# Kernel optimization log

Hardware: AMD Instinct MI355X
Metric: run time of the kernel (lower is better)

## Reference

```python
import jax, jax.numpy as jnp
import numpy as np

D, H, F, N, V, B, S, T = 512, 8, 2048, 2, 32000, 2, 1024, 1024


def _pe(seq_len, d):
    pos = np.arange(seq_len)[:, None].astype(np.float32)
    div = np.exp(np.arange(0, d, 2).astype(np.float32) * (-np.log(10000.0) / d))
    pe = np.zeros((seq_len, d), np.float32)
    pe[:, 0::2] = np.sin(pos * div)
    pe[:, 1::2] = np.cos(pos * div)
    return jnp.asarray(pe)


def _ln(x, g, b, eps=1e-6):
    # torch .var() default is unbiased (ddof=1)
    m = x.mean(-1, keepdims=True)
    v = jnp.sum((x - m) ** 2, -1, keepdims=True) / (x.shape[-1] - 1)
    return g * (x - m) / jnp.sqrt(v + eps) + b


def _mha(q, k, v, mask, w, b):
    # w: [4, D, D] (q,k,v,o); b: [4, D]
    Bq, Sq, Dm = q.shape
    Sk = k.shape[1]
    dk = Dm // H
    Q = (q @ w[0] + b[0]).reshape(Bq, Sq, H, dk).transpose(0, 2, 1, 3)
    K = (k @ w[1] + b[1]).reshape(Bq, Sk, H, dk).transpose(0, 2, 1, 3)
    Vv = (v @ w[2] + b[2]).reshape(Bq, Sk, H, dk).transpose(0, 2, 1, 3)
    s = jnp.einsum('bhqd,bhkd->bhqk', Q, K) / jnp.sqrt(jnp.float32(dk))
    s = jnp.where(mask == 0, jnp.float32(-1e9), s)
    a = jax.nn.softmax(s, axis=-1)
    o = jnp.einsum('bhqk,bhkd->bhqd', a, Vv).transpose(0, 2, 1, 3).reshape(Bq, Sq, Dm)
    return o @ w[3] + b[3]


def _ffn(x, w1, b1, w2, b2):
    return jax.nn.relu(x @ w1 + b1) @ w2 + b2


def _forward(src, tgt, src_mask, tgt_mask, p):
    (src_emb, tgt_emb, ea_w, ea_b, ef_w1, ef_b1, ef_w2, ef_b2, eln_g, eln_b, en_g, en_b,
     ds_w, ds_b, dc_w, dc_b, df_w1, df_b1, df_w2, df_b2, dln_g, dln_b, dn_g, dn_b, pw, pb) = p
    scale = jnp.sqrt(jnp.float32(D))
    # encoder
    x = src_emb[src] * scale + _pe(src.shape[1], D)
    for i in range(N):
        h = _ln(x, eln_g[i, 0], eln_b[i, 0])
        x = x + _mha(h, h, h, src_mask, ea_w[i], ea_b[i])
        h = _ln(x, eln_g[i, 1], eln_b[i, 1])
        x = x + _ffn(h, ef_w1[i], ef_b1[i], ef_w2[i], ef_b2[i])
    enc = _ln(x, en_g, en_b)
    # decoder
    y = tgt_emb[tgt] * scale + _pe(tgt.shape[1], D)
    for i in range(N):
        h = _ln(y, dln_g[i, 0], dln_b[i, 0])
        y = y + _mha(h, h, h, tgt_mask, ds_w[i], ds_b[i])
        h = _ln(y, dln_g[i, 1], dln_b[i, 1])
        y = y + _mha(h, enc, enc, src_mask, dc_w[i], dc_b[i])
        h = _ln(y, dln_g[i, 2], dln_b[i, 2])
        y = y + _ffn(h, df_w1[i], df_b1[i], df_w2[i], df_b2[i])
    y = _ln(y, dn_g, dn_b)
    return jax.nn.log_softmax(y @ pw + pb, axis=-1)


def setup_inputs() -> dict:
    key = jax.random.key(0)
    c = [0]
    def nk():
        c[0] += 1
        return jax.random.fold_in(key, c[0])
    def w(*s):
        return jax.random.normal(nk(), s, jnp.float32) * 0.02
    inp = {
        'src': jax.random.randint(nk(), (B, S), 0, V, jnp.int32),
        'tgt': jax.random.randint(nk(), (B, T), 0, V, jnp.int32),
        'src_mask': jnp.ones((B, 1, 1, S), jnp.int32),
        'tgt_mask': jnp.tril(jnp.ones((T, T), jnp.int32))[None, None],
        'src_emb': w(V, D), 'tgt_emb': w(V, D),
        'enc_attn_w': w(N, 4, D, D), 'enc_attn_b': jnp.zeros((N, 4, D), jnp.float32),
        'enc_ffn_w1': w(N, D, F), 'enc_ffn_b1': jnp.zeros((N, F), jnp.float32),
        'enc_ffn_w2': w(N, F, D), 'enc_ffn_b2': jnp.zeros((N, D), jnp.float32),
        'enc_ln_g': jnp.ones((N, 2, D), jnp.float32), 'enc_ln_b': jnp.zeros((N, 2, D), jnp.float32),
        'enc_norm_g': jnp.ones((D,), jnp.float32), 'enc_norm_b': jnp.zeros((D,), jnp.float32),
        'dec_self_w': w(N, 4, D, D), 'dec_self_b': jnp.zeros((N, 4, D), jnp.float32),
        'dec_cross_w': w(N, 4, D, D), 'dec_cross_b': jnp.zeros((N, 4, D), jnp.float32),
        'dec_ffn_w1': w(N, D, F), 'dec_ffn_b1': jnp.zeros((N, F), jnp.float32),
        'dec_ffn_w2': w(N, F, D), 'dec_ffn_b2': jnp.zeros((N, D), jnp.float32),
        'dec_ln_g': jnp.ones((N, 3, D), jnp.float32), 'dec_ln_b': jnp.zeros((N, 3, D), jnp.float32),
        'dec_norm_g': jnp.ones((D,), jnp.float32), 'dec_norm_b': jnp.zeros((D,), jnp.float32),
        'proj_w': w(D, V), 'proj_b': jnp.zeros((V,), jnp.float32),
    }
    return inp


def reference(src, tgt, src_mask, tgt_mask, src_emb, tgt_emb, enc_attn_w, enc_attn_b,
              enc_ffn_w1, enc_ffn_b1, enc_ffn_w2, enc_ffn_b2, enc_ln_g, enc_ln_b,
              enc_norm_g, enc_norm_b, dec_self_w, dec_self_b, dec_cross_w, dec_cross_b,
              dec_ffn_w1, dec_ffn_b1, dec_ffn_w2, dec_ffn_b2, dec_ln_g, dec_ln_b,
              dec_norm_g, dec_norm_b, proj_w, proj_b):
    p = (src_emb, tgt_emb, enc_attn_w, enc_attn_b, enc_ffn_w1, enc_ffn_b1, enc_ffn_w2,
         enc_ffn_b2, enc_ln_g, enc_ln_b, enc_norm_g, enc_norm_b, dec_self_w, dec_self_b,
         dec_cross_w, dec_cross_b, dec_ffn_w1, dec_ffn_b1, dec_ffn_w2, dec_ffn_b2,
         dec_ln_g, dec_ln_b, dec_norm_g, dec_norm_b, proj_w, proj_b)
    return _forward(src, tgt, src_mask, tgt_mask, p)
```

## Files before the change

kernel.cpp:

```cpp
#include <hip/hip_runtime.h>
#include <hip/hip_bf16.h>
#include <math.h>

using bf16 = __hip_bfloat16;
typedef float f32x4 __attribute__((ext_vector_type(4)));
typedef short short8 __attribute__((ext_vector_type(8)));

constexpr int kD = 512, kH = 8, kDk = 64, kF = 2048, kV = 32000;
constexpr int kB = 2, kS = 1024, kM = 2048, kBH = 16;

enum { ST_F32 = 0, ST_BF16, ST_QKV };

__device__ __forceinline__ void gload_lds16(const void* g, void* l) {
  __builtin_amdgcn_global_load_lds(
      (const __attribute__((address_space(1))) void*)g,
      (__attribute__((address_space(3))) void*)l, 16, 0, 0);
}

__device__ __forceinline__ float bfu2f(short u) {
  union { unsigned int i; float f; } c;
  c.i = ((unsigned int)(unsigned short)u) << 16;
  return c.f;
}

template <int BM, int BN, int STM, bool BIAS, bool RELU, bool RES, int NBUF, bool XSWZ, bool ASEL>
__launch_bounds__(256)
__global__ void k_gemm(const bf16* __restrict__ A, int lda, long long Az,
                       const bf16* __restrict__ Bt, int ldb, long long Bz,
                       void* __restrict__ Cv, int ldc, long long Cz,
                       int K, float alpha,
                       const float* __restrict__ bias,
                       const float* __restrict__ res,
                       const bf16* __restrict__ A2) {
  static_assert(NBUF == 1 || (BM == 64 && BN == 64), "pipeline path sized for 64x64");
  constexpr int FM = BM / 32, FN = BN / 32;
  __shared__ __attribute__((aligned(16))) bf16 As[NBUF][BM * 64];
  __shared__ __attribute__((aligned(16))) bf16 Bs[NBUF][BN * 64];
  const int tid = threadIdx.x;
  const int w = tid >> 6, lane = tid & 63;
  int bx = blockIdx.x, by = blockIdx.y;
  if constexpr (XSWZ) {
    const int nx = gridDim.x, ny = gridDim.y;
    const int lin = by * nx + bx;
    const int cpx = (nx * ny) >> 3;
    const int s = (lin & 7) * cpx + (lin >> 3);
    bx = s / ny;
    by = s - bx * ny;
  }
  const int bm = by * BM, bn = bx * BN;
  const int z = blockIdx.z;
  if constexpr (ASEL) { if (bn >= 512) A = A2; }
  A += (long long)z * Az;
  Bt += (long long)z * Bz;
  const int l15 = lane & 15, lhi = lane >> 4;
  const int wr = (w >> 1) * (BM / 2), wc = (w & 1) * (BN / 2);
  f32x4 acc[FM][FN] = {};
  const int nkt = K >> 6;

  auto stage = [&](int kt, int nb) {
#pragma unroll
    for (int it = 0; it < BM / 32; ++it) {
      int chunk = (it * 4 + w) * 64 + lane;
      int row = chunk >> 3, c = chunk & 7;
      int col = (c ^ (row & 7)) << 3;
      gload_lds16(A + (size_t)(bm + row) * lda + kt * 64 + col, As[nb] + (it * 4 + w) * 512);
    }
#pragma unroll
    for (int it = 0; it < BN / 32; ++it) {
      int chunk = (it * 4 + w) * 64 + lane;
      int row = chunk >> 3, c = chunk & 7;
      int col = (c ^ (row & 7)) << 3;
      gload_lds16(Bt + (size_t)(bn + row) * ldb + kt * 64 + col, Bs[nb] + (it * 4 + w) * 512);
    }
  };
  auto compute = [&](int cb) {
#pragma unroll
    for (int kk = 0; kk < 2; ++kk) {
      short8 af[FM], bf[FN];
#pragma unroll
      for (int i = 0; i < FM; ++i) {
        int row = wr + i * 16 + l15;
        af[i] = *(const short8*)(As[cb] + row * 64 + (((kk * 4 + lhi) ^ (row & 7)) * 8));
      }
#pragma unroll
      for (int j = 0; j < FN; ++j) {
        int row = wc + j * 16 + l15;
        bf[j] = *(const short8*)(Bs[cb] + row * 64 + (((kk * 4 + lhi) ^ (row & 7)) * 8));
      }
#pragma unroll
      for (int i = 0; i < FM; ++i)
#pragma unroll
        for (int j = 0; j < FN; ++j)
          acc[i][j] = __builtin_amdgcn_mfma_f32_16x16x32_bf16(af[i], bf[j], acc[i][j], 0, 0, 0);
    }
  };

  if constexpr (NBUF == 3) {
    stage(0, 0);
    stage(1, 1);
    stage(2, 2);
    asm volatile("s_waitcnt vmcnt(8)" ::: "memory");
    __builtin_amdgcn_s_barrier();
    __builtin_amdgcn_sched_barrier(0);
    int cur = 0;
    for (int kt = 0; kt < nkt; ++kt) {
      compute(cur);
      asm volatile("s_waitcnt lgkmcnt(0)" ::: "memory");
      __builtin_amdgcn_sched_barrier(0);
      if (kt + 1 < nkt) {
        __builtin_amdgcn_s_barrier();
        if (kt + 3 < nkt) {
          stage(kt + 3, cur);
          asm volatile("s_waitcnt vmcnt(8)" ::: "memory");
        } else {
          asm volatile("s_waitcnt vmcnt(0)" ::: "memory");
        }
        __builtin_amdgcn_s_barrier();
        __builtin_amdgcn_sched_barrier(0);
      }
      cur = (cur == 2) ? 0 : cur + 1;
    }
  } else {
    for (int kt = 0; kt < nkt; ++kt) {
      stage(kt, 0);
      __syncthreads();
      compute(0);
      __syncthreads();
    }
  }

#pragma unroll
  for (int i = 0; i < FM; ++i) {
#pragma unroll
    for (int j = 0; j < FN; ++j) {
#pragma unroll
      for (int r = 0; r < 4; ++r) {
        int m = bm + wr + i * 16 + lhi * 4 + r;
        int n = bn + wc + j * 16 + l15;
        float val = acc[i][j][r] * alpha;
        if constexpr (BIAS) val += bias[n];
        if constexpr (RELU) val = fmaxf(val, 0.f);
        if constexpr (RES) val += res[(size_t)m * ldc + n];
        if constexpr (STM == ST_F32) {
          ((float*)Cv)[(size_t)z * Cz + (size_t)m * ldc + n] = val;
        } else if constexpr (STM == ST_BF16) {
          ((bf16*)Cv)[(size_t)z * Cz + (size_t)m * ldc + n] = __float2bfloat16(val);
        } else if constexpr (STM == ST_QKV) {
          int seg = n >> 9, nn = n & 511;
          int b_ = m >> 10, s_ = m & 1023, h_ = nn >> 6, d_ = nn & 63;
          size_t idx = (seg < 2)
              ? (((size_t)(b_ * kH + h_) << 10) + s_) * kDk + d_
              : ((size_t)(b_ * kH + h_) * kDk + d_) * kS + s_;
          ((bf16*)Cv)[(size_t)seg * 1048576 + idx] = __float2bfloat16(val);
        }
      }
    }
  }
}

template <bool CAUSAL>
__launch_bounds__(256)
__global__ void k_fattn(const bf16* __restrict__ Q, const bf16* __restrict__ K,
                        const bf16* __restrict__ Vt, bf16* __restrict__ O) {
  __shared__ __attribute__((aligned(16))) bf16 Ks[3][4096];
  __shared__ __attribute__((aligned(16))) bf16 Vs[3][4096];
  __shared__ __attribute__((aligned(16))) bf16 Ps[4][1024];
  const int tid = threadIdx.x, w = tid >> 6, lane = tid & 63;
  const int l15 = lane & 15, lhi = lane >> 4;
  const int q0 = blockIdx.x * 64, bh = blockIdx.y;
  const int qw = q0 + w * 16;
  const bf16* Qp = Q + (((size_t)(bh << 10)) + qw + l15) * kDk;
  short8 aq[2];
  aq[0] = *(const short8*)(Qp + lhi * 8);
  aq[1] = *(const short8*)(Qp + 32 + lhi * 8);
  const int srow = w * 8 + (lane >> 3);
  const int sc = (lane & 7) ^ (srow & 7);
  const bf16* Ksrc = K + (((size_t)(bh << 10)) + srow) * kDk + sc * 8;
  const bf16* Vsrc = Vt + ((size_t)bh * kDk + srow) * kS + sc * 8;
  const int nt = CAUSAL ? (q0 >> 6) + 1 : (kS >> 6);

  auto stage = [&](int t, int nb) {
    int kv0 = t << 6;
    gload_lds16(Ksrc + (size_t)kv0 * kDk, Ks[nb] + w * 512);
    gload_lds16(Ksrc + (size_t)(kv0 + 32) * kDk, Ks[nb] + 2048 + w * 512);
    gload_lds16(Vsrc + kv0, Vs[nb] + w * 512);
    gload_lds16(Vsrc + kv0 + 32 * kS, Vs[nb] + 2048 + w * 512);
  };

  float m_[4], l_[4];
#pragma unroll
  for (int r = 0; r < 4; ++r) { m_[r] = -1e30f; l_[r] = 0.f; }
  f32x4 ao[4] = {};

  stage(0, 0);
  if (nt > 2) {
    stage(1, 1);
    stage(2, 2);
    asm volatile("s_waitcnt vmcnt(8)" ::: "memory");
  } else if (nt > 1) {
    stage(1, 1);
    asm volatile("s_waitcnt vmcnt(4)" ::: "memory");
  } else {
    asm volatile("s_waitcnt vmcnt(0)" ::: "memory");
  }
  __builtin_amdgcn_s_barrier();
  __builtin_amdgcn_sched_barrier(0);

  int cur = 0;
  for (int t = 0; t < nt; ++t) {
    f32x4 as[4] = {};
#pragma unroll
    for (int kk = 0; kk < 2; ++kk) {
      short8 bk[4];
#pragma unroll
      for (int nf = 0; nf < 4; ++nf) {
        int row = nf * 16 + l15;
        int c = (4 * kk + lhi) ^ (row & 7);
        bk[nf] = *(const short8*)(Ks[cur] + row * 64 + c * 8);
      }
#pragma unroll
      for (int nf = 0; nf < 4; ++nf)
        as[nf] = __builtin_amdgcn_mfma_f32_16x16x32_bf16(aq[kk], bk[nf], as[nf], 0, 0, 0);
    }
    float s[4][4];
#pragma unroll
    for (int nf = 0; nf < 4; ++nf)
#pragma unroll
      for (int r = 0; r < 4; ++r) {
        float v = as[nf][r] * 0.125f;
        if (CAUSAL && t == nt - 1) {
          int col = (t << 6) + nf * 16 + l15;
          int row = qw + lhi * 4 + r;
          if (col > row) v = -1e30f;
        }
        s[nf][r] = v;
      }
    float mn[4], scl[4], rsum[4];
#pragma unroll
    for (int r = 0; r < 4; ++r) {
      float mx = fmaxf(fmaxf(s[0][r], s[1][r]), fmaxf(s[2][r], s[3][r]));
      mx = fmaxf(mx, __shfl_xor(mx, 1));
      mx = fmaxf(mx, __shfl_xor(mx, 2));
      mx = fmaxf(mx, __shfl_xor(mx, 4));
      mx = fmaxf(mx, __shfl_xor(mx, 8));
      mn[r] = fmaxf(m_[r], mx);
      scl[r] = __expf(m_[r] - mn[r]);
      rsum[r] = 0.f;
    }
#pragma unroll
    for (int nf = 0; nf < 4; ++nf)
#pragma unroll
      for (int r = 0; r < 4; ++r) {
        float p = __expf(s[nf][r] - mn[r]);
        rsum[r] += p;
        int pr = lhi * 4 + r;
        int c = (2 * nf + (l15 >> 3)) ^ (pr & 7);
        Ps[w][pr * 64 + c * 8 + (l15 & 7)] = __float2bfloat16(p);
      }
#pragma unroll
    for (int r = 0; r < 4; ++r) {
      float su = rsum[r];
      su += __shfl_xor(su, 1);
      su += __shfl_xor(su, 2);
      su += __shfl_xor(su, 4);
      su += __shfl_xor(su, 8);
      l_[r] = l_[r] * scl[r] + su;
      m_[r] = mn[r];
    }
#pragma unroll
    for (int nf = 0; nf < 4; ++nf)
#pragma unroll
      for (int r = 0; r < 4; ++r) ao[nf][r] *= scl[r];
    asm volatile("s_waitcnt lgkmcnt(0)" ::: "memory");
    __builtin_amdgcn_sched_barrier(0);
#pragma unroll
    for (int kk = 0; kk < 2; ++kk) {
      short8 pa = *(const short8*)(Ps[w] + l15 * 64 + (((4 * kk + lhi) ^ (l15 & 7)) * 8));
      short8 bv[4];
#pragma unroll
      for (int nf = 0; nf < 4; ++nf) {
        int row = nf * 16 + l15;
        int c = (4 * kk + lhi) ^ (row & 7);
        bv[nf] = *(const short8*)(Vs[cur] + row * 64 + c * 8);
      }
#pragma unroll
      for (int nf = 0; nf < 4; ++nf)
        ao[nf] = __builtin_amdgcn_mfma_f32_16x16x32_bf16(pa, bv[nf], ao[nf], 0, 0, 0);
    }
    asm volatile("s_waitcnt lgkmcnt(0)" ::: "memory");
    __builtin_amdgcn_sched_barrier(0);
    if (t + 1 < nt) {
      __builtin_amdgcn_s_barrier();
      if (t + 3 < nt) {
        stage(t + 3, cur);
        asm volatile("s_waitcnt vmcnt(8)" ::: "memory");
      } else {
        asm volatile("s_waitcnt vmcnt(0)" ::: "memory");
      }
      __builtin_amdgcn_s_barrier();
      __builtin_amdgcn_sched_barrier(0);
    }
    cur = (cur == 2) ? 0 : cur + 1;
  }
  const int b_ = bh >> 3, h_ = bh & 7;
  float inv[4];
#pragma unroll
  for (int r = 0; r < 4; ++r) inv[r] = 1.f / l_[r];
#pragma unroll
  for (int nf = 0; nf < 4; ++nf)
#pragma unroll
    for (int r = 0; r < 4; ++r) {
      int q = qw + lhi * 4 + r;
      O[((size_t)(b_ * kS + q)) * kD + h_ * kDk + nf * 16 + l15] =
          __float2bfloat16(ao[nf][r] * inv[r]);
    }
}

struct TJobs {
  const float* src[8];
  bf16* dst[8];
  int K[8], N[8];
  int ofs[9];
};

__global__ void k_transpose_all(TJobs J) {
  __shared__ float t[32][33];
  const int tb = blockIdx.x;
  int j = 0;
#pragma unroll
  for (int i = 1; i < 8; ++i) j += (tb >= J.ofs[i]) ? 1 : 0;
  const int K = J.K[j], N = J.N[j];
  const int tn = N >> 5, tk = K >> 5;
  int r = tb - J.ofs[j];
  const int z = r / (tn * tk);
  r -= z * tn * tk;
  const int k0 = (r / tn) << 5, n0 = (r % tn) << 5;
  const float* Wp = J.src[j] + (size_t)z * K * N;
  bf16* WTp = J.dst[j] + (size_t)z * K * N;
  const int tx = threadIdx.x, ty = threadIdx.y;
#pragma unroll
  for (int rr = 0; rr < 32; rr += 8) t[ty + rr][tx] = Wp[(size_t)(k0 + ty + rr) * N + n0 + tx];
  __syncthreads();
#pragma unroll
  for (int rr = 0; rr < 32; rr += 8)
    WTp[(size_t)(n0 + ty + rr) * K + k0 + tx] = __float2bfloat16(t[tx][ty + rr]);
}

__global__ void k_embed2(const int* __restrict__ src, const int* __restrict__ tgt,
                         const float* __restrict__ se, const float* __restrict__ te,
                         float* __restrict__ xe, float* __restrict__ xd) {
  const int m = blockIdx.x, which = blockIdx.y;
  const int* tok = which ? tgt : src;
  const float* emb = which ? te : se;
  float* x = which ? xd : xe;
  int s = m & (kS - 1);
  const float* e = emb + (size_t)tok[m] * kD;
  float* xp = x + (size_t)m * kD;
  for (int d = threadIdx.x; d < kD; d += 256) {
    int i = d >> 1;
    float freq = __expf(-(float)(2 * i) * (9.210340371976184f / 512.0f));
    float ang = (float)s * freq;
    float pe = (d & 1) ? cosf(ang) : sinf(ang);
    xp[d] = e[d] * 22.62741699796952f + pe;
  }
}

__global__ void k_ln(const float* __restrict__ x, const float* __restrict__ g,
                     const float* __restrict__ b, bf16* __restrict__ out) {
  int w = threadIdx.x >> 6, lane = threadIdx.x & 63;
  int row = blockIdx.x * 4 + w;
  const float* xp = x + (size_t)row * kD;
  float v[8];
  float sum = 0.f;
#pragma unroll
  for (int i = 0; i < 8; ++i) { v[i] = xp[lane + i * 64]; sum += v[i]; }
#pragma unroll
  for (int o = 32; o; o >>= 1) sum += __shfl_xor(sum, o);
  float mean = sum * (1.f / 512.f);
  float sq = 0.f;
#pragma unroll
  for (int i = 0; i < 8; ++i) { float d = v[i] - mean; sq += d * d; }
#pragma unroll
  for (int o = 32; o; o >>= 1) sq += __shfl_xor(sq, o);
  float inv = rsqrtf(sq * (1.f / 511.f) + 1e-6f);
  bf16* op = out + (size_t)row * kD;
#pragma unroll
  for (int i = 0; i < 8; ++i) {
    int d = lane + i * 64;
    op[d] = __float2bfloat16(g[d] * (v[i] - mean) * inv + b[d]);
  }
}

__global__ __launch_bounds__(512, 1) void k_proj256(const bf16* __restrict__ A,
                                                    const bf16* __restrict__ Bt,
                                                    bf16* __restrict__ C,
                                                    const float* __restrict__ bias) {
  __shared__ __attribute__((aligned(16))) bf16 As[4][256 * 32];
  __shared__ __attribute__((aligned(16))) bf16 Bs[4][256 * 32];
  const int tid = threadIdx.x, w = tid >> 6, lane = tid & 63;
  const int l15 = lane & 15, lhi = lane >> 4;
  const int lin = blockIdx.y * 125 + blockIdx.x;
  const int s = (lin & 7) * 125 + (lin >> 3);
  const int bx = s >> 3, by = s & 7;
  const int bm = by * 256, bn = bx * 256;
  const int wr = (w >> 2) * 128, wc = (w & 3) * 64;
  const int rowq = tid >> 2, chk = tid & 3;
  const int swz = (chk ^ ((rowq >> 1) & 3)) << 3;
  const bf16* Asrc0 = A + (size_t)(bm + rowq) * kD + swz;
  const bf16* Asrc1 = A + (size_t)(bm + 128 + rowq) * kD + swz;
  const bf16* Bsrc0 = Bt + (size_t)(bn + rowq) * kD + swz;
  const bf16* Bsrc1 = Bt + (size_t)(bn + 128 + rowq) * kD + swz;
  const int ldsoff = w * 1024;

  auto stage = [&](int kt) {
    const int b = kt & 3;
    const int ko = kt * 32;
    gload_lds16(Asrc0 + ko, (char*)As[b] + ldsoff);
    gload_lds16(Asrc1 + ko, (char*)As[b] + 8192 + ldsoff);
    gload_lds16(Bsrc0 + ko, (char*)Bs[b] + ldsoff);
    gload_lds16(Bsrc1 + ko, (char*)Bs[b] + 8192 + ldsoff);
  };

  const int ra = wr + l15, rb = wc + l15;
  const int abase = ra * 64 + ((lhi ^ ((ra >> 1) & 3)) << 4);
  const int bbase = rb * 64 + ((lhi ^ ((rb >> 1) & 3)) << 4);

  f32x4 acc[8][4] = {};
  stage(0); stage(1); stage(2);
  for (int kt = 0; kt < 16; ++kt) {
    if (kt + 2 < 16)      asm volatile("s_waitcnt vmcnt(8)" ::: "memory");
    else if (kt + 1 < 16) asm volatile("s_waitcnt vmcnt(4)" ::: "memory");
    else                  asm volatile("s_waitcnt vmcnt(0)" ::: "memory");
    __builtin_amdgcn_s_barrier();
    __builtin_amdgcn_sched_barrier(0);
    if (kt + 3 < 16) stage(kt + 3);
    const int b = kt & 3;
    short8 af[8], bf[4];
#pragma unroll
    for (int i = 0; i < 8; ++i)
      af[i] = *(const short8*)((const char*)As[b] + abase + i * 1024);
#pragma unroll
    for (int j = 0; j < 4; ++j)
      bf[j] = *(const short8*)((const char*)Bs[b] + bbase + j * 1024);
#pragma unroll
    for (int i = 0; i < 8; ++i)
#pragma unroll
      for (int j = 0; j < 4; ++j)
        acc[i][j] = __builtin_amdgcn_mfma_f32_16x16x32_bf16(af[i], bf[j], acc[i][j], 0, 0, 0);
    asm volatile("s_waitcnt lgkmcnt(0)" ::: "memory");
    __builtin_amdgcn_sched_barrier(0);
  }
#pragma unroll
  for (int i = 0; i < 8; ++i)
#pragma unroll
    for (int j = 0; j < 4; ++j)
#pragma unroll
      for (int r = 0; r < 4; ++r) {
        int m = bm + wr + i * 16 + lhi * 4 + r;
        int n = bn + wc + j * 16 + l15;
        C[(size_t)m * kV + n] = __float2bfloat16(acc[i][j][r] + bias[n]);
      }
}

__global__ __launch_bounds__(640, 2) void k_lsm_bf(const bf16* __restrict__ L,
                                                   float* __restrict__ y) {
  const bf16* row = L + (size_t)blockIdx.x * kV;
  float* orow = y + (size_t)blockIdx.x * kV;
  const int t = threadIdx.x;
  const bool extra = t < 160;
  float v[56];
  float sum = 0.f;
#pragma unroll
  for (int i = 0; i < 6; ++i) {
    short8 s = *(const short8*)(row + (t + i * 640) * 8);
#pragma unroll
    for (int e = 0; e < 8; ++e) {
      float f = bfu2f(s[e]);
      v[i * 8 + e] = f;
      sum += __expf(f);
    }
  }
  if (extra) {
    short8 s = *(const short8*)(row + (3840 + t) * 8);
#pragma unroll
    for (int e = 0; e < 8; ++e) {
      float f = bfu2f(s[e]);
      v[48 + e] = f;
      sum += __expf(f);
    }
  }
#pragma unroll
  for (int o = 32; o; o >>= 1) sum += __shfl_xor(sum, o);
  __shared__ float red2[10];
  const int w = t >> 6, lane = t & 63;
  if (lane == 0) red2[w] = sum;
  __syncthreads();
  sum = 0.f;
#pragma unroll
  for (int i = 0; i < 10; ++i) sum += red2[i];
  const float sh = logf(sum);
#pragma unroll
  for (int i = 0; i < 6; ++i)
#pragma unroll
    for (int e = 0; e < 8; ++e) orow[(t + i * 640) * 8 + e] = v[i * 8 + e] - sh;
  if (extra)
#pragma unroll
    for (int e = 0; e < 8; ++e) orow[(3840 + t) * 8 + e] = v[48 + e] - sh;
}

extern "C" void kernel_launch(void* const* d_in, const int* in_sizes, int n_in,
                              void* d_out, int out_size, void* d_ws, size_t ws_size,
                              hipStream_t stream) {
  (void)in_sizes; (void)n_in; (void)out_size;
  if (ws_size < (size_t)212 * 1024 * 1024) return;

  const int* src = (const int*)d_in[0];
  const int* tgt = (const int*)d_in[1];
  const float* src_emb   = (const float*)d_in[4];
  const float* tgt_emb   = (const float*)d_in[5];
  const float* enc_attn_w = (const float*)d_in[6];
  const float* enc_attn_b = (const float*)d_in[7];
  const float* enc_ffn_w1 = (const float*)d_in[8];
  const float* enc_ffn_b1 = (const float*)d_in[9];
  const float* enc_ffn_w2 = (const float*)d_in[10];
  const float* enc_ffn_b2 = (const float*)d_in[11];
  const float* enc_ln_g  = (const float*)d_in[12];
  const float* enc_ln_b  = (const float*)d_in[13];
  const float* enc_norm_g = (const float*)d_in[14];
  const float* enc_norm_b = (const float*)d_in[15];
  const float* dec_self_w = (const float*)d_in[16];
  const float* dec_self_b = (const float*)d_in[17];
  const float* dec_cross_w = (const float*)d_in[18];
  const float* dec_cross_b = (const float*)d_in[19];
  const float* dec_ffn_w1 = (const float*)d_in[20];
  const float* dec_ffn_b1 = (const float*)d_in[21];
  const float* dec_ffn_w2 = (const float*)d_in[22];
  const float* dec_ffn_b2 = (const float*)d_in[23];
  const float* dec_ln_g  = (const float*)d_in[24];
  const float* dec_ln_b  = (const float*)d_in[25];
  const float* dec_norm_g = (const float*)d_in[26];
  const float* dec_norm_b = (const float*)d_in[27];
  const float* proj_w    = (const float*)d_in[28];
  const float* proj_b    = (const float*)d_in[29];

  char* ws = (char*)d_ws;
  auto MB = [](size_t x) { return x << 20; };
  bf16* enc_attn_wt  = (bf16*)(ws + MB(0));
  bf16* dec_self_wt  = (bf16*)(ws + MB(4));
  bf16* dec_cross_wt = (bf16*)(ws + MB(8));
  bf16* enc_f1t = (bf16*)(ws + MB(12));
  bf16* enc_f2t = (bf16*)(ws + MB(16));
  bf16* dec_f1t = (bf16*)(ws + MB(20));
  bf16* dec_f2t = (bf16*)(ws + MB(24));
  bf16* proj_wt = (bf16*)(ws + MB(28));
  float* x_enc  = (float*)(ws + MB(60));
  float* x_dec  = (float*)(ws + MB(64));
  bf16* hbuf    = (bf16*)(ws + MB(68));
  bf16* enc_bf  = (bf16*)(ws + MB(70));
  bf16* Qb      = (bf16*)(ws + MB(72));
  bf16* attn_o  = (bf16*)(ws + MB(78));
  bf16* logits  = (bf16*)(ws + MB(80));
  bf16* ffn_mid = (bf16*)d_out;

  TJobs tj;
  int acc = 0;
  auto setj = [&](int j, const float* s, bf16* d, int K, int N, int z) {
    tj.src[j] = s; tj.dst[j] = d; tj.K[j] = K; tj.N[j] = N; tj.ofs[j] = acc;
    acc += (K >> 5) * (N >> 5) * z;
  };
  setj(0, enc_attn_w, enc_attn_wt, 512, 512, 8);
  setj(1, dec_self_w, dec_self_wt, 512, 512, 8);
  setj(2, dec_cross_w, dec_cross_wt, 512, 512, 8);
  setj(3, enc_ffn_w1, enc_f1t, 512, 2048, 2);
  setj(4, enc_ffn_w2, enc_f2t, 2048, 512, 2);
  setj(5, dec_ffn_w1, dec_f1t, 512, 2048, 2);
  setj(6, dec_ffn_w2, dec_f2t, 2048, 512, 2);
  setj(7, proj_w, proj_wt, 512, 32000, 1);
  tj.ofs[8] = acc;
  k_transpose_all<<<acc, dim3(32, 8), 0, stream>>>(tj);

  k_embed2<<<dim3(kM, 2), 256, 0, stream>>>(src, tgt, src_emb, tgt_emb, x_enc, x_dec);

  auto LN = [&](const float* x, const float* g, const float* b, bf16* out) {
    k_ln<<<kM / 4, 256, 0, stream>>>(x, g, b, out);
  };
  auto out_proj = [&](const bf16* wt, const float* bias, float* xio) {
    k_gemm<64, 64, ST_F32, true, false, true, 3, false, false><<<dim3(8, 32, 1), 256, 0, stream>>>(
        attn_o, 512, 0, wt + 3 * 262144, 512, 0, xio, 512, 0, 512, 1.f, bias + 3 * 512, xio, nullptr);
  };
  auto self_attn = [&](const bf16* wt, const float* bias, bool causal, float* xio) {
    k_gemm<64, 64, ST_QKV, true, false, false, 3, false, false><<<dim3(24, 32, 1), 256, 0, stream>>>(
        hbuf, 512, 0, wt, 512, 0, Qb, 0, 0, 512, 1.f, bias, nullptr, nullptr);
    if (causal) k_fattn<true><<<dim3(16, kBH), 256, 0, stream>>>(Qb, Qb + 1048576, Qb + 2097152, attn_o);
    else        k_fattn<false><<<dim3(16, kBH), 256, 0, stream>>>(Qb, Qb + 1048576, Qb + 2097152, attn_o);
    out_proj(wt, bias, xio);
  };
  auto cross_attn = [&](const bf16* wt, const float* bias, float* xio) {
    k_gemm<64, 64, ST_QKV, true, false, false, 3, false, true><<<dim3(24, 32, 1), 256, 0, stream>>>(
        hbuf, 512, 0, wt, 512, 0, Qb, 0, 0, 512, 1.f, bias, nullptr, enc_bf);
    k_fattn<false><<<dim3(16, kBH), 256, 0, stream>>>(Qb, Qb + 1048576, Qb + 2097152, attn_o);
    out_proj(wt, bias, xio);
  };
  auto ffn_block = [&](float* xio, const bf16* w1t, const float* b1, const bf16* w2t,
                       const float* b2, const float* g, const float* bl) {
    LN(xio, g, bl, hbuf);
    k_gemm<64, 64, ST_BF16, true, true, false, 3, false, false><<<dim3(32, 32, 1), 256, 0, stream>>>(
        hbuf, 512, 0, w1t, 512, 0, ffn_mid, kF, 0, 512, 1.f, b1, nullptr, nullptr);
    k_gemm<64, 64, ST_F32, true, false, true, 3, false, false><<<dim3(8, 32, 1), 256, 0, stream>>>(
        ffn_mid, 2048, 0, w2t, 2048, 0, xio, 512, 0, 2048, 1.f, b2, xio, nullptr);
  };

  for (int i = 0; i < 2; ++i) {
    LN(x_enc, enc_ln_g + i * 1024, enc_ln_b + i * 1024, hbuf);
    self_attn(enc_attn_wt + (size_t)i * 1048576, enc_attn_b + i * 2048, false, x_enc);
    ffn_block(x_enc, enc_f1t + (size_t)i * 1048576, enc_ffn_b1 + i * 2048,
              enc_f2t + (size_t)i * 1048576, enc_ffn_b2 + i * 512,
              enc_ln_g + i * 1024 + 512, enc_ln_b + i * 1024 + 512);
  }
  LN(x_enc, enc_norm_g, enc_norm_b, enc_bf);

  for (int i = 0; i < 2; ++i) {
    LN(x_dec, dec_ln_g + i * 1536, dec_ln_b + i * 1536, hbuf);
    self_attn(dec_self_wt + (size_t)i * 1048576, dec_self_b + i * 2048, true, x_dec);
    LN(x_dec, dec_ln_g + i * 1536 + 512, dec_ln_b + i * 1536 + 512, hbuf);
    cross_attn(dec_cross_wt + (size_t)i * 1048576, dec_cross_b + i * 2048, x_dec);
    ffn_block(x_dec, dec_f1t + (size_t)i * 1048576, dec_ffn_b1 + i * 2048,
              dec_f2t + (size_t)i * 1048576, dec_ffn_b2 + i * 512,
              dec_ln_g + i * 1536 + 1024, dec_ln_b + i * 1536 + 1024);
  }
  LN(x_dec, dec_norm_g, dec_norm_b, hbuf);

  k_proj256<<<dim3(125, 8), 512, 0, stream>>>(hbuf, proj_wt, logits, proj_b);
  k_lsm_bf<<<kM, 640, 0, stream>>>(logits, (float*)d_out);
}
```

Measured before the change: 690.9 us.

## Fuse LayerNorm into residual GEMM epilogues and merge prep kernels

Each residual-output GEMM (attention out-projection and FFN down-projection) now counts finished column tiles per row block with an atomic counter. The last block to finish a row panel runs the following LayerNorm on those 64 rows, which removes the standalone LN launches. The weight transpose, embedding, and first encoder/decoder LayerNorms are merged into one prep kernel, with a second hbuf so the decoder's first LN can be done up front. The cost is a threadfence and atomic per block, a serialized LN tail on the last block of each row panel, and a memset for the counters.

```diff
diff --git a/kernel.cpp b/kernel.cpp
--- a/kernel.cpp
+++ b/kernel.cpp
@@ -23,7 +23,36 @@
   return c.f;
 }
 
-template <int BM, int BN, int STM, bool BIAS, bool RELU, bool RES, int NBUF, bool XSWZ, bool ASEL>
+__device__ __forceinline__ void ln4(int vb, const float* __restrict__ x,
+                                    const float* __restrict__ g,
+                                    const float* __restrict__ b,
+                                    bf16* __restrict__ out) {
+  int w = threadIdx.x >> 6, lane = threadIdx.x & 63;
+  int row = vb * 4 + w;
+  const float* xp = x + (size_t)row * kD;
+  float v[8];
+  float sum = 0.f;
+#pragma unroll
+  for (int i = 0; i < 8; ++i) { v[i] = xp[lane + i * 64]; sum += v[i]; }
+#pragma unroll
+  for (int o = 32; o; o >>= 1) sum += __shfl_xor(sum, o);
+  float mean = sum * (1.f / 512.f);
+  float sq = 0.f;
+#pragma unroll
+  for (int i = 0; i < 8; ++i) { float d = v[i] - mean; sq += d * d; }
+#pragma unroll
+  for (int o = 32; o; o >>= 1) sq += __shfl_xor(sq, o);
+  float inv = rsqrtf(sq * (1.f / 511.f) + 1e-6f);
+  bf16* op = out + (size_t)row * kD;
+#pragma unroll
+  for (int i = 0; i < 8; ++i) {
+    int d = lane + i * 64;
+    op[d] = __float2bfloat16(g[d] * (v[i] - mean) * inv + b[d]);
+  }
+}
+
+template <int BM, int BN, int STM, bool BIAS, bool RELU, bool RES, int NBUF, bool XSWZ,
+          bool ASEL, bool FUSELN>
 __launch_bounds__(256)
 __global__ void k_gemm(const bf16* __restrict__ A, int lda, long long Az,
                        const bf16* __restrict__ Bt, int ldb, long long Bz,
@@ -31,7 +60,11 @@
                        int K, float alpha,
                        const float* __restrict__ bias,
                        const float* __restrict__ res,
-                       const bf16* __restrict__ A2) {
+                       const bf16* __restrict__ A2,
+                       const float* __restrict__ lng,
+                       const float* __restrict__ lnb,
+                       bf16* __restrict__ lnout,
+                       unsigned* __restrict__ cnt) {
   static_assert(NBUF == 1 || (BM == 64 && BN == 64), "pipeline path sized for 64x64");
   constexpr int FM = BM / 32, FN = BN / 32;
   __shared__ __attribute__((aligned(16))) bf16 As[NBUF][BM * 64];
@@ -156,6 +189,23 @@
       }
     }
   }
+
+  if constexpr (FUSELN) {
+    __threadfence();
+    __syncthreads();
+    __shared__ int lastf;
+    if (tid == 0) {
+      unsigned v = __hip_atomic_fetch_add(&cnt[blockIdx.y], 1u,
+                                          __ATOMIC_ACQ_REL, __HIP_MEMORY_SCOPE_AGENT);
+      lastf = (v == gridDim.x - 1u) ? 1 : 0;
+    }
+    __syncthreads();
+    if (lastf) {
+      const float* xsrc = (const float*)Cv;
+#pragma unroll
+      for (int i = 0; i < BM / 4; ++i) ln4((bm >> 2) + i, xsrc, lng, lnb, lnout);
+    }
+  }
 }
 
 template <bool CAUSAL>
@@ -323,71 +373,83 @@
   int ofs[9];
 };
 
-__global__ void k_transpose_all(TJobs J) {
+struct PrepArgs {
+  TJobs tj; int ntile;
+  const int *src, *tgt;
+  const float *src_emb, *tgt_emb;
+  const float *eg, *eb, *dg, *db;
+  float *x_enc, *x_dec;
+  bf16 *hb_enc, *hb_dec;
+};
+
+__global__ void k_prep(PrepArgs P) {
   __shared__ float t[32][33];
-  const int tb = blockIdx.x;
-  int j = 0;
-#pragma unroll
-  for (int i = 1; i < 8; ++i) j += (tb >= J.ofs[i]) ? 1 : 0;
-  const int K = J.K[j], N = J.N[j];
-  const int tn = N >> 5, tk = K >> 5;
-  int r = tb - J.ofs[j];
-  const int z = r / (tn * tk);
-  r -= z * tn * tk;
-  const int k0 = (r / tn) << 5, n0 = (r % tn) << 5;
-  const float* Wp = J.src[j] + (size_t)z * K * N;
-  bf16* WTp = J.dst[j] + (size_t)z * K * N;
-  const int tx = threadIdx.x, ty = threadIdx.y;
-#pragma unroll
-  for (int rr = 0; rr < 32; rr += 8) t[ty + rr][tx] = Wp[(size_t)(k0 + ty + rr) * N + n0 + tx];
-  __syncthreads();
-#pragma unroll
-  for (int rr = 0; rr < 32; rr += 8)
-    WTp[(size_t)(n0 + ty + rr) * K + k0 + tx] = __float2bfloat16(t[tx][ty + rr]);
-}
-
-__global__ void k_embed2(const int* __restrict__ src, const int* __restrict__ tgt,
-                         const float* __restrict__ se, const float* __restrict__ te,
-                         float* __restrict__ xe, float* __restrict__ xd) {
-  const int m = blockIdx.x, which = blockIdx.y;
-  const int* tok = which ? tgt : src;
-  const float* emb = which ? te : se;
-  float* x = which ? xd : xe;
-  int s = m & (kS - 1);
+  __shared__ float red[4], red2[4];
+  const int tid = threadIdx.x;
+  if ((int)blockIdx.x < P.ntile) {
+    const int tb = blockIdx.x;
+    int j = 0;
+#pragma unroll
+    for (int i = 1; i < 8; ++i) j += (tb >= P.tj.ofs[i]) ? 1 : 0;
+    const int K = P.tj.K[j], N = P.tj.N[j];
+    const int tn = N >> 5, tk = K >> 5;
+    int r = tb - P.tj.ofs[j];
+    const int z = r / (tn * tk);
+    r -= z * tn * tk;
+    const int k0 = (r / tn) << 5, n0 = (r % tn) << 5;
+    const float* Wp = P.tj.src[j] + (size_t)z * K * N;
+    bf16* WTp = P.tj.dst[j] + (size_t)z * K * N;
+    const int tx = tid & 31, ty = tid >> 5;
+#pragma unroll
+    for (int rr = 0; rr < 32; rr += 8)
+      t[ty + rr][tx] = Wp[(size_t)(k0 + ty + rr) * N + n0 + tx];
+    __syncthreads();
+#pragma unroll
+    for (int rr = 0; rr < 32; rr += 8)
+      WTp[(size_t)(n0 + ty + rr) * K + k0 + tx] = __float2bfloat16(t[tx][ty + rr]);
+    return;
+  }
+  const int vb = blockIdx.x - P.ntile;
+  const int m = vb & (kM - 1), which = vb >> 11;
+  const int* tok = which ? P.tgt : P.src;
+  const float* emb = which ? P.tgt_emb : P.src_emb;
+  float* x = which ? P.x_dec : P.x_enc;
+  const int s = m & (kS - 1);
   const float* e = emb + (size_t)tok[m] * kD;
   float* xp = x + (size_t)m * kD;
-  for (int d = threadIdx.x; d < kD; d += 256) {
+  float v[2];
+#pragma unroll
+  for (int h = 0; h < 2; ++h) {
+    int d = tid + h * 256;
     int i = d >> 1;
     float freq = __expf(-(float)(2 * i) * (9.210340371976184f / 512.0f));
     float ang = (float)s * freq;
     float pe = (d & 1) ? cosf(ang) : sinf(ang);
-    xp[d] = e[d] * 22.62741699796952f + pe;
-  }
-}
-
-__global__ void k_ln(const float* __restrict__ x, const float* __restrict__ g,
-                     const float* __restrict__ b, bf16* __restrict__ out) {
-  int w = threadIdx.x >> 6, lane = threadIdx.x & 63;
-  int row = blockIdx.x * 4 + w;
-  const float* xp = x + (size_t)row * kD;
-  float v[8];
-  float sum = 0.f;
-#pragma unroll
-  for (int i = 0; i < 8; ++i) { v[i] = xp[lane + i * 64]; sum += v[i]; }
+    v[h] = e[d] * 22.62741699796952f + pe;
+    xp[d] = v[h];
+  }
+  const int w = tid >> 6, lane = tid & 63;
+  float sum = v[0] + v[1];
 #pragma unroll
   for (int o = 32; o; o >>= 1) sum += __shfl_xor(sum, o);
-  float mean = sum * (1.f / 512.f);
-  float sq = 0.f;
-#pragma unroll
-  for (int i = 0; i < 8; ++i) { float d = v[i] - mean; sq += d * d; }
+  if (lane == 0) red[w] = sum;
+  __syncthreads();
+  sum = red[0] + red[1] + red[2] + red[3];
+  const float mean = sum * (1.f / 512.f);
+  float sq = (v[0] - mean) * (v[0] - mean) + (v[1] - mean) * (v[1] - mean);
 #pragma unroll
   for (int o = 32; o; o >>= 1) sq += __shfl_xor(sq, o);
-  float inv = rsqrtf(sq * (1.f / 511.f) + 1e-6f);
-  bf16* op = out + (size_t)row * kD;
-#pragma unroll
-  for (int i = 0; i < 8; ++i) {
-    int d = lane + i * 64;
-    op[d] = __float2bfloat16(g[d] * (v[i] - mean) * inv + b[d]);
+  if (lane == 0) red2[w] = sq;
+  __syncthreads();
+  sq = red2[0] + red2[1] + red2[2] + red2[3];
+  const float rstd = rsqrtf(sq * (1.f / 511.f) + 1e-6f);
+  const float* g = which ? P.dg : P.eg;
+  const float* b = which ? P.db : P.eb;
+  bf16* hb = (which ? P.hb_dec : P.hb_enc) + (size_t)m * kD;
+#pragma unroll
+  for (int h = 0; h < 2; ++h) {
+    int d = tid + h * 256;
+    hb[d] = __float2bfloat16(g[d] * (v[h] - mean) * rstd + b[d]);
   }
 }
 
@@ -560,12 +622,14 @@
   bf16* Qb      = (bf16*)(ws + MB(72));
   bf16* attn_o  = (bf16*)(ws + MB(78));
   bf16* logits  = (bf16*)(ws + MB(80));
+  unsigned* cntbase = (unsigned*)(ws + MB(206));
+  bf16* hbuf2   = (bf16*)(ws + MB(208));
   bf16* ffn_mid = (bf16*)d_out;
 
-  TJobs tj;
+  PrepArgs P;
   int acc = 0;
   auto setj = [&](int j, const float* s, bf16* d, int K, int N, int z) {
-    tj.src[j] = s; tj.dst[j] = d; tj.K[j] = K; tj.N[j] = N; tj.ofs[j] = acc;
+    P.tj.src[j] = s; P.tj.dst[j] = d; P.tj.K[j] = K; P.tj.N[j] = N; P.tj.ofs[j] = acc;
     acc += (K >> 5) * (N >> 5) * z;
   };
   setj(0, enc_attn_w, enc_attn_wt, 512, 512, 8);
@@ -576,59 +640,84 @@
   setj(5, dec_ffn_w1, dec_f1t, 512, 2048, 2);
   setj(6, dec_ffn_w2, dec_f2t, 2048, 512, 2);
   setj(7, proj_w, proj_wt, 512, 32000, 1);
-  tj.ofs[8] = acc;
-  k_transpose_all<<<acc, dim3(32, 8), 0, stream>>>(tj);
-
-  k_embed2<<<dim3(kM, 2), 256, 0, stream>>>(src, tgt, src_emb, tgt_emb, x_enc, x_dec);
-
-  auto LN = [&](const float* x, const float* g, const float* b, bf16* out) {
-    k_ln<<<kM / 4, 256, 0, stream>>>(x, g, b, out);
-  };
-  auto out_proj = [&](const bf16* wt, const float* bias, float* xio) {
-    k_gemm<64, 64, ST_F32, true, false, true, 3, false, false><<<dim3(8, 32, 1), 256, 0, stream>>>(
-        attn_o, 512, 0, wt + 3 * 262144, 512, 0, xio, 512, 0, 512, 1.f, bias + 3 * 512, xio, nullptr);
-  };
-  auto self_attn = [&](const bf16* wt, const float* bias, bool causal, float* xio) {
-    k_gemm<64, 64, ST_QKV, true, false, false, 3, false, false><<<dim3(24, 32, 1), 256, 0, stream>>>(
-        hbuf, 512, 0, wt, 512, 0, Qb, 0, 0, 512, 1.f, bias, nullptr, nullptr);
+  P.tj.ofs[8] = acc;
+  P.ntile = acc;
+  P.src = src; P.tgt = tgt;
+  P.src_emb = src_emb; P.tgt_emb = tgt_emb;
+  P.eg = enc_ln_g; P.eb = enc_ln_b;
+  P.dg = dec_ln_g; P.db = dec_ln_b;
+  P.x_enc = x_enc; P.x_dec = x_dec;
+  P.hb_enc = hbuf; P.hb_dec = hbuf2;
+
+  hipMemsetAsync(cntbase, 0, 1280, stream);
+  k_prep<<<acc + 2 * kM, 256, 0, stream>>>(P);
+
+  int slice = 0;
+  auto out_proj_ln = [&](const bf16* wt, const float* bias, float* xio,
+                         const float* lg, const float* lb, bf16* lnout) {
+    k_gemm<64, 64, ST_F32, true, false, true, 3, false, false, true>
+        <<<dim3(8, 32, 1), 256, 0, stream>>>(
+        attn_o, 512, 0, wt + 3 * 262144, 512, 0, xio, 512, 0, 512, 1.f,
+        bias + 3 * 512, xio, nullptr, lg, lb, lnout, cntbase + (slice++) * 32);
+  };
+  auto qkv = [&](const bf16* aptr, const bf16* wt, const float* bias, const bf16* kvA) {
+    if (kvA)
+      k_gemm<64, 64, ST_QKV, true, false, false, 3, false, true, false>
+          <<<dim3(24, 32, 1), 256, 0, stream>>>(
+          aptr, 512, 0, wt, 512, 0, Qb, 0, 0, 512, 1.f, bias, nullptr, kvA,
+          nullptr, nullptr, nullptr, nullptr);
+    else
+      k_gemm<64, 64, ST_QKV, true, false, false, 3, false, false, false>
+          <<<dim3(24, 32, 1), 256, 0, stream>>>(
+          aptr, 512, 0, wt, 512, 0, Qb, 0, 0, 512, 1.f, bias, nullptr, nullptr,
+          nullptr, nullptr, nullptr, nullptr);
+  };
+  auto fattn = [&](bool causal) {
     if (causal) k_fattn<true><<<dim3(16, kBH), 256, 0, stream>>>(Qb, Qb + 1048576, Qb + 2097152, attn_o);
     else        k_fattn<false><<<dim3(16, kBH), 256, 0, stream>>>(Qb, Qb + 1048576, Qb + 2097152, attn_o);
-    out_proj(wt, bias, xio);
-  };
-  auto cross_attn = [&](const bf16* wt, const float* bias, float* xio) {
-    k_gemm<64, 64, ST_QKV, true, false, false, 3, false, true><<<dim3(24, 32, 1), 256, 0, stream>>>(
-        hbuf, 512, 0, wt, 512, 0, Qb, 0, 0, 512, 1.f, bias, nullptr, enc_bf);
-    k_fattn<false><<<dim3(16, kBH), 256, 0, stream>>>(Qb, Qb + 1048576, Qb + 2097152, attn_o);
-    out_proj(wt, bias, xio);
-  };
-  auto ffn_block = [&](float* xio, const bf16* w1t, const float* b1, const bf16* w2t,
-                       const float* b2, const float* g, const float* bl) {
-    LN(xio, g, bl, hbuf);
-    k_gemm<64, 64, ST_BF16, true, true, false, 3, false, false><<<dim3(32, 32, 1), 256, 0, stream>>>(
-        hbuf, 512, 0, w1t, 512, 0, ffn_mid, kF, 0, 512, 1.f, b1, nullptr, nullptr);
-    k_gemm<64, 64, ST_F32, true, false, true, 3, false, false><<<dim3(8, 32, 1), 256, 0, stream>>>(
-        ffn_mid, 2048, 0, w2t, 2048, 0, xio, 512, 0, 2048, 1.f, b2, xio, nullptr);
+  };
+  auto ffn = [&](float* xio, const bf16* w1t, const float* b1, const bf16* w2t,
+                 const float* b2, const float* lg, const float* lb, bf16* lnout) {
+    k_gemm<64, 64, ST_BF16, true, true, false, 3, false, false, false>
+        <<<dim3(32, 32, 1), 256, 0, stream>>>(
+        hbuf, 512, 0, w1t, 512, 0, ffn_mid, kF, 0, 512, 1.f, b1, nullptr, nullptr,
+        nullptr, nullptr, nullptr, nullptr);
+    k_gemm<64, 64, ST_F32, true, false, true, 3, false, false, true>
+        <<<dim3(8, 32, 1), 256, 0, stream>>>(
+        ffn_mid, 2048, 0, w2t, 2048, 0, xio, 512, 0, 2048, 1.f, b2, xio, nullptr,
+        lg, lb, lnout, cntbase + (slice++) * 32);
   };
 
   for (int i = 0; i < 2; ++i) {
-    LN(x_enc, enc_ln_g + i * 1024, enc_ln_b + i * 1024, hbuf);
-    self_attn(enc_attn_wt + (size_t)i * 1048576, enc_attn_b + i * 2048, false, x_enc);
-    ffn_block(x_enc, enc_f1t + (size_t)i * 1048576, enc_ffn_b1 + i * 2048,
-              enc_f2t + (size_t)i * 1048576, enc_ffn_b2 + i * 512,
-              enc_ln_g + i * 1024 + 512, enc_ln_b + i * 1024 + 512);
-  }
-  LN(x_enc, enc_norm_g, enc_norm_b, enc_bf);
+    const bf16* wt = enc_attn_wt + (size_t)i * 1048576;
+    const float* bias = enc_attn_b + i * 2048;
+    qkv(hbuf, wt, bias, nullptr);
+    fattn(false);
+    out_proj_ln(wt, bias, x_enc, enc_ln_g + i * 1024 + 512, enc_ln_b + i * 1024 + 512, hbuf);
+    const float* ng = (i == 0) ? enc_ln_g + 1024 : enc_norm_g;
+    const float* nb = (i == 0) ? enc_ln_b + 1024 : enc_norm_b;
+    bf16* nout = (i == 0) ? hbuf : enc_bf;
+    ffn(x_enc, enc_f1t + (size_t)i * 1048576, enc_ffn_b1 + i * 2048,
+        enc_f2t + (size_t)i * 1048576, enc_ffn_b2 + i * 512, ng, nb, nout);
+  }
 
   for (int i = 0; i < 2; ++i) {
-    LN(x_dec, dec_ln_g + i * 1536, dec_ln_b + i * 1536, hbuf);
-    self_attn(dec_self_wt + (size_t)i * 1048576, dec_self_b + i * 2048, true, x_dec);
-    LN(x_dec, dec_ln_g + i * 1536 + 512, dec_ln_b + i * 1536 + 512, hbuf);
-    cross_attn(dec_cross_wt + (size_t)i * 1048576, dec_cross_b + i * 2048, x_dec);
-    ffn_block(x_dec, dec_f1t + (size_t)i * 1048576, dec_ffn_b1 + i * 2048,
-              dec_f2t + (size_t)i * 1048576, dec_ffn_b2 + i * 512,
-              dec_ln_g + i * 1536 + 1024, dec_ln_b + i * 1536 + 1024);
-  }
-  LN(x_dec, dec_norm_g, dec_norm_b, hbuf);
+    const bf16* wts = dec_self_wt + (size_t)i * 1048576;
+    const float* bs = dec_self_b + i * 2048;
+    const bf16* wtc = dec_cross_wt + (size_t)i * 1048576;
+    const float* bc = dec_cross_b + i * 2048;
+    qkv((i == 0) ? hbuf2 : hbuf, wts, bs, nullptr);
+    fattn(true);
+    out_proj_ln(wts, bs, x_dec, dec_ln_g + i * 1536 + 512, dec_ln_b + i * 1536 + 512, hbuf);
+    qkv(hbuf, wtc, bc, enc_bf);
+    fattn(false);
+    out_proj_ln(wtc, bc, x_dec, dec_ln_g + i * 1536 + 1024, dec_ln_b + i * 1536 + 1024, hbuf);
+    const float* ng = (i == 0) ? dec_ln_g + 1536 : dec_norm_g;
+    const float* nb = (i == 0) ? dec_ln_b + 1536 : dec_norm_b;
+    ffn(x_dec, dec_f1t + (size_t)i * 1048576, dec_ffn_b1 + i * 2048,
+        dec_f2t + (size_t)i * 1048576, dec_ffn_b2 + i * 512, ng, nb, hbuf);
+    (void)ng; (void)nb;
+  }
 
   k_proj256<<<dim3(125, 8), 512, 0, stream>>>(hbuf, proj_wt, logits, proj_b);
   k_lsm_bf<<<kM, 640, 0, stream>>>(logits, (float*)d_out);
```

After: 1.031 ms. +49.2%, slower.
